# Optimization experiments

Hardware: AMD Instinct MI355X
Metric: run time of the kernel (lower is better)

Reference implementation:

```python
import jax, jax.numpy as jnp
import numpy as np

N_NODES = 10000
N_EDGES = 160000
IN_F = 256
CH = 512
N_LABELS = 1440


def setup_inputs() -> dict:
    key = jax.random.key(0)
    ks = jax.random.split(key, 12)
    x = jax.random.normal(ks[0], (N_NODES, IN_F), dtype=jnp.float32)
    src = jax.random.randint(ks[1], (N_EDGES,), 0, N_NODES)
    dst = jax.random.randint(ks[2], (N_EDGES,), 0, N_NODES)
    s_in = 1.0 / np.sqrt(IN_F)
    s_ch = 1.0 / np.sqrt(CH)
    W1 = jax.random.normal(ks[3], (IN_F, CH), dtype=jnp.float32) * s_in
    V1 = jax.random.normal(ks[4], (IN_F, CH), dtype=jnp.float32) * s_in
    b1 = jnp.zeros((CH,), dtype=jnp.float32)
    Wk = jax.random.normal(ks[5], (6, CH, CH), dtype=jnp.float32) * s_ch
    Vk = jax.random.normal(ks[6], (6, CH, CH), dtype=jnp.float32) * s_ch
    bk = jnp.zeros((6, CH), dtype=jnp.float32)
    Wd = jax.random.normal(ks[7], (CH, N_LABELS), dtype=jnp.float32) * s_ch
    bd = jnp.zeros((N_LABELS,), dtype=jnp.float32)
    return {"x": x, "src": src, "dst": dst, "W1": W1, "V1": V1, "b1": b1,
            "Wk": Wk, "Vk": Vk, "bk": bk, "Wd": Wd, "bd": bd}


def reference(x, src, dst, W1, V1, b1, Wk, Vk, bk, Wd, bd):
    n = x.shape[0]
    ones = jnp.ones(src.shape[0], dtype=x.dtype)
    # degree-normalized adjacency weights: D_out^{-1/2} A D_in^{-1/2}
    deg_out = jnp.maximum(jax.ops.segment_sum(ones, src, num_segments=n), 1.0)
    deg_in = jnp.maximum(jax.ops.segment_sum(ones, dst, num_segments=n), 1.0)
    w = jax.lax.rsqrt(deg_out[src] * deg_in[dst])  # [E]

    def arma_conv(h, W, V, b):
        m = h @ W                                      # dense transform [N, CH]
        msg = w[:, None] * m[dst]                      # gather + scale   [E, CH]
        agg = jax.ops.segment_sum(msg, src, num_segments=n)  # scatter   [N, CH]
        # gcn_activation relu then outer activation relu (idempotent)
        return jax.nn.relu(agg + h @ V + b)

    h = arma_conv(x, W1, V1, b1)
    for i in range(6):  # convs 2..7, fixed small layer count
        h = arma_conv(h, Wk[i], Vk[i], bk[i])
    return h @ Wd + bd
```

## Files before the change

kernel.cpp:

```cpp
#include <hip/hip_runtime.h>
#include <hip/hip_bf16.h>
#include <stdint.h>

#define NN 10000
#define NE 160000
#define INF 256
#define CH 512
#define NL 1440
#define MPAN 158

typedef __bf16 bf16;
typedef __attribute__((ext_vector_type(8))) bf16 bf16x8;
typedef __attribute__((ext_vector_type(4))) float f32x4;


__device__ __forceinline__ void gload16(const void* g, const void* l) {
    auto gp = reinterpret_cast<const __attribute__((address_space(1))) uint32_t*>(
        reinterpret_cast<uintptr_t>(g));
    auto lp = reinterpret_cast<__attribute__((address_space(3))) uint32_t*>(
        reinterpret_cast<uintptr_t>(l));
    __builtin_amdgcn_global_load_lds(gp, lp, 16, 0, 0);
}

__global__ void deg_kernel(const int* __restrict__ src, const int* __restrict__ dst,
                           int* __restrict__ deg_out, int* __restrict__ deg_in) {
    int e = blockIdx.x * 256 + threadIdx.x;
    if (e < NE) {
        atomicAdd(&deg_out[src[e]], 1);
        atomicAdd(&deg_in[dst[e]], 1);
    }
}

__global__ __launch_bounds__(1024) void scan_kernel(const int* __restrict__ deg,
                                                    int* __restrict__ offsets,
                                                    int* __restrict__ cursor) {
    __shared__ int sums[1024];
    const int PER = 10;
    int tid = threadIdx.x;
    int base = tid * PER;
    int local[PER];
    int s = 0;
    #pragma unroll
    for (int i = 0; i < PER; i++) {
        int v = (base + i < NN) ? deg[base + i] : 0;
        local[i] = s;
        s += v;
    }
    sums[tid] = s;
    __syncthreads();
    for (int off = 1; off < 1024; off <<= 1) {
        int v = (tid >= off) ? sums[tid - off] : 0;
        __syncthreads();
        sums[tid] += v;
        __syncthreads();
    }
    int prev = (tid > 0) ? sums[tid - 1] : 0;
    #pragma unroll
    for (int i = 0; i < PER; i++) {
        if (base + i < NN) {
            int o = prev + local[i];
            offsets[base + i] = o;
            cursor[base + i] = o;
        }
    }
    if (tid == 0) offsets[NN] = sums[1023];
}

__global__ void csr_kernel(const int* __restrict__ src, const int* __restrict__ dst,
                           const int* __restrict__ deg_out, const int* __restrict__ deg_in,
                           int* __restrict__ cursor, int2* __restrict__ edge_pk) {
    int e = blockIdx.x * 256 + threadIdx.x;
    if (e < NE) {
        int s = src[e], d = dst[e];
        float dw = (float)max(deg_out[s], 1) * (float)max(deg_in[d], 1);
        float w = rsqrtf(dw);
        int pos = atomicAdd(&cursor[s], 1);
        edge_pk[pos] = make_int2(d, __float_as_int(w));
    }
}

__global__ __launch_bounds__(256) void gather_agg(
    const uint32_t* __restrict__ h32,
    const int* __restrict__ offsets,
    const int2* __restrict__ edge_pk,
    bf16* __restrict__ outA,
    int CHU, int SLOG, int CBASE, int PANCH) {
    int p = blockIdx.x;
    int slice = p & ((1 << SLOG) - 1);
    int grp = p >> SLOG;
    int wid = threadIdx.x >> 6;
    int lane = threadIdx.x & 63;
    int u = grp * 4 + wid;
    if (u >= NN) return;
    int c = slice * 128 + lane * 2;
    int cu = (slice << 6) + lane;

    int beg = offsets[u], end = offsets[u + 1];
    float a0 = 0.f, a1 = 0.f;
    int e = beg;
    for (; e + 3 < end; e += 4) {
        int2 p0 = edge_pk[e], p1 = edge_pk[e + 1];
        int2 p2 = edge_pk[e + 2], p3 = edge_pk[e + 3];
        uint32_t q0 = h32[p0.x * CHU + cu];
        uint32_t q1 = h32[p1.x * CHU + cu];
        uint32_t q2 = h32[p2.x * CHU + cu];
        uint32_t q3 = h32[p3.x * CHU + cu];
        float w0 = __int_as_float(p0.y), w1 = __int_as_float(p1.y);
        float w2 = __int_as_float(p2.y), w3 = __int_as_float(p3.y);
        a0 += w0 * __uint_as_float(q0 << 16);
        a1 += w0 * __uint_as_float(q0 & 0xffff0000u);
        a0 += w1 * __uint_as_float(q1 << 16);
        a1 += w1 * __uint_as_float(q1 & 0xffff0000u);
        a0 += w2 * __uint_as_float(q2 << 16);
        a1 += w2 * __uint_as_float(q2 & 0xffff0000u);
        a0 += w3 * __uint_as_float(q3 << 16);
        a1 += w3 * __uint_as_float(q3 & 0xffff0000u);
    }
    for (; e < end; e++) {
        int2 pe = edge_pk[e];
        uint32_t qv = h32[pe.x * CHU + cu];
        float wt = __int_as_float(pe.y);
        a0 += wt * __uint_as_float(qv << 16);
        a1 += wt * __uint_as_float(qv & 0xffff0000u);
    }

    bf16 h0 = (bf16)a0, h1 = (bf16)a1;
    int row = u & 63, panel = u >> 6;
    int ch = CBASE + (c >> 5), g = (c >> 3) & 3, j = c & 7;
    size_t base = (size_t)panel * PANCH * 2048 + (size_t)ch * 2048 + g * 512 + row * 8 + j;
    uint32_t hw = (uint32_t)__builtin_bit_cast(uint16_t, h0) |
                  ((uint32_t)__builtin_bit_cast(uint16_t, h1) << 16);
    *(uint32_t*)&outA[base] = hw;
}

__global__ void xb_conv(const float* __restrict__ x, bf16* __restrict__ xb) {
    int idx = blockIdx.x * 256 + threadIdx.x;
    if (idx >= NN * 32) return;
    const float* src = x + (size_t)idx * 8;
    float4 v0 = *(const float4*)src;
    float4 v1 = *(const float4*)(src + 4);
    bf16x8 o;
    o[0] = (bf16)v0.x; o[1] = (bf16)v0.y; o[2] = (bf16)v0.z; o[3] = (bf16)v0.w;
    o[4] = (bf16)v1.x; o[5] = (bf16)v1.y; o[6] = (bf16)v1.z; o[7] = (bf16)v1.w;
    *(bf16x8*)&xb[(size_t)idx * 8] = o;
}

__global__ void split_hi(const float* __restrict__ in, bf16* __restrict__ out,
                         int M, int K, int PANCH) {
    int idx = blockIdx.x * 256 + threadIdx.x;
    int K8 = K >> 3;
    if (idx >= M * K8) return;
    int m = idx / K8;
    int k8 = (idx % K8) * 8;
    bf16x8 hi;
    #pragma unroll
    for (int j = 0; j < 8; j++) hi[j] = (bf16)in[(size_t)m * K + k8 + j];
    int panel = m >> 6, row = m & 63;
    int c = k8 >> 5, g = (k8 & 31) >> 3;
    size_t base = ((size_t)panel * PANCH + c) * 2048 + g * 512 + row * 8;
    *(bf16x8*)&out[base] = hi;
}

__global__ void vw_split(const float* __restrict__ V, const float* __restrict__ W,
                         bf16* __restrict__ out, int K,
                         size_t vStride, size_t wStride, size_t outStride) {
    int z = blockIdx.z;
    V += (size_t)z * vStride;
    W += (size_t)z * wStride;
    out += (size_t)z * outStride;
    int idx = blockIdx.x * 256 + threadIdx.x;
    int K8 = K >> 3;
    if (idx >= 512 * K8) return;
    int k8 = (idx / 512) * 8;
    int n = idx % 512;
    int KCh = K >> 5;
    bf16x8 vv, ww;
    #pragma unroll
    for (int j = 0; j < 8; j++) {
        vv[j] = (bf16)V[(size_t)(k8 + j) * 512 + n];
        ww[j] = (bf16)W[(size_t)(k8 + j) * 512 + n];
    }
    int panel = n >> 7, row = n & 127;
    int c = k8 >> 5, g = (k8 & 31) >> 3;
    size_t base = (size_t)panel * (2 * KCh) * 4096 + g * 1024 + row * 8;
    *(bf16x8*)&out[base + (size_t)c * 4096] = vv;
    *(bf16x8*)&out[base + (size_t)(KCh + c) * 4096] = ww;
}

__global__ void tsplit(const float* __restrict__ in, bf16* __restrict__ out,
                       int K, int N) {
    int idx = blockIdx.x * 256 + threadIdx.x;
    int K8 = K >> 3;
    if (idx >= N * K8) return;
    int k8 = (idx / N) * 8;
    int n = idx % N;
    int KCh = K >> 5;
    bf16x8 hi;
    #pragma unroll
    for (int j = 0; j < 8; j++) hi[j] = (bf16)in[(size_t)(k8 + j) * N + n];
    int panel = n >> 7, row = n & 127;
    int c = k8 >> 5, g = (k8 & 31) >> 3;
    size_t base = ((size_t)panel * KCh) * 4096 + g * 1024 + row * 8;
    *(bf16x8*)&out[base + (size_t)c * 4096] = hi;
}

__global__ __launch_bounds__(256, 3) void gemm_layer(
    const bf16* __restrict__ At, const bf16* __restrict__ Bt,
    const float* __restrict__ bias, bf16* __restrict__ hbOut,
    bf16* __restrict__ AtNext, int M, int KCh, int BX) {
    __shared__ bf16 lA[2][2][2048];
    __shared__ bf16 lB[2][2][4096];

    int nwg = gridDim.x;
    int q = nwg >> 3, r = nwg & 7;
    int p = blockIdx.x;
    int xcd = p & 7, slot = p >> 3;
    int L = (xcd < r ? xcd * (q + 1) : r * (q + 1) + (xcd - r) * q) + slot;
    int by = L / BX, bx = L % BX;

    int tid = threadIdx.x;
    int lane = tid & 63, w = tid >> 6;
    int wm = w >> 1, wn = w & 1;
    int lr = lane & 15, lg = lane >> 4;
    const bf16* Ab = At + (size_t)by * KCh * 2048;
    const bf16* Bb = Bt + (size_t)bx * KCh * 4096;

    f32x4 acc[2][4];
    #pragma unroll
    for (int i = 0; i < 2; i++)
        #pragma unroll
        for (int j = 0; j < 4; j++) {
            f32x4 z = {0.f, 0.f, 0.f, 0.f};
            acc[i][j] = z;
        }

    int u0 = tid, u1 = tid + 256;
    int offA = lg * 512 + (wm * 32 + lr) * 8;
    int offB = lg * 1024 + (wn * 64 + lr) * 8;

    #define LSTAGE(bufi, it)                                                      \
        do {                                                                      \
            const bf16* a0 = Ab + (size_t)(2 * (it)) * 2048;                      \
            const bf16* a1 = Ab + (size_t)(2 * (it) + 1) * 2048;                  \
            const bf16* b0 = Bb + (size_t)(2 * (it)) * 4096;                      \
            const bf16* b1 = Bb + (size_t)(2 * (it) + 1) * 4096;                  \
            gload16(a0 + tid * 8, &lA[bufi][0][tid * 8]);                         \
            gload16(a1 + tid * 8, &lA[bufi][1][tid * 8]);                         \
            gload16(b0 + u0 * 8, &lB[bufi][0][u0 * 8]);                           \
            gload16(b0 + u1 * 8, &lB[bufi][0][u1 * 8]);                           \
            gload16(b1 + u0 * 8, &lB[bufi][1][u0 * 8]);                           \
            gload16(b1 + u1 * 8, &lB[bufi][1][u1 * 8]);                           \
        } while (0)

    int NIT = KCh >> 1;
    LSTAGE(0, 0);
    __syncthreads();

    int buf = 0;
    for (int it = 0; it < NIT; it++) {
        if (it + 1 < NIT) LSTAGE(buf ^ 1, it + 1);
        #pragma unroll
        for (int kk = 0; kk < 2; kk++) {
            bf16x8 bh[4];
            #pragma unroll
            for (int n = 0; n < 4; n++)
                bh[n] = *(const bf16x8*)&lB[buf][kk][offB + n * 128];
            #pragma unroll
            for (int m = 0; m < 2; m++) {
                bf16x8 ah = *(const bf16x8*)&lA[buf][kk][offA + m * 128];
                #pragma unroll
                for (int n = 0; n < 4; n++)
                    acc[m][n] = __builtin_amdgcn_mfma_f32_16x16x32_bf16(
                        ah, bh[n], acc[m][n], 0, 0, 0);
            }
        }
        __syncthreads();
        buf ^= 1;
    }
    #undef LSTAGE

    int m0 = by * 64, n0 = bx * 128;
    #pragma unroll
    for (int m = 0; m < 2; m++) {
        #pragma unroll
        for (int n = 0; n < 4; n++) {
            int gr0 = m0 + wm * 32 + m * 16 + lg * 4;
            int gc = n0 + wn * 64 + n * 16 + lr;
            float bv = bias[gc];
            int cch = gc >> 5, g2 = (gc >> 3) & 3, j2 = gc & 7;
            #pragma unroll
            for (int r2 = 0; r2 < 4; r2++) {
                int grow = gr0 + r2;
                if (grow >= M) continue;
                float v = fmaxf(acc[m][n][r2] + bv, 0.f);
                bf16 hv = (bf16)v;
                hbOut[(size_t)grow * 512 + gc] = hv;
                int panel = grow >> 6, row = grow & 63;
                AtNext[(size_t)panel * 32 * 2048 + (size_t)cch * 2048 +
                       g2 * 512 + row * 8 + j2] = hv;
            }
        }
    }
}

__global__ __launch_bounds__(256, 4) void gemm_out(
    const bf16* __restrict__ At, const bf16* __restrict__ Bt,
    float* __restrict__ Fout, const float* __restrict__ bias,
    int M, int N, int KCh, int BX, int PANCH) {
    __shared__ bf16 ldsA[2][2][2048];
    __shared__ bf16 ldsB[2][4096];

    int nwg = gridDim.x;
    int q = nwg >> 3, r = nwg & 7;
    int p = blockIdx.x;
    int xcd = p & 7, slot = p >> 3;
    int L = (xcd < r ? xcd * (q + 1) : r * (q + 1) + (xcd - r) * q) + slot;
    int by = L / BX, bx = L % BX;

    int tid = threadIdx.x;
    int lane = tid & 63, w = tid >> 6;
    int wm = w >> 1, wn = w & 1;
    int lr = lane & 15, lg = lane >> 4;
    const bf16* Ab0 = At + (size_t)(2 * by) * PANCH * 2048;
    const bf16* Ab1 = At + (size_t)(2 * by + 1) * PANCH * 2048;
    const bf16* Bbase = Bt + (size_t)bx * KCh * 4096;

    f32x4 acc[4][4];
    #pragma unroll
    for (int i = 0; i < 4; i++)
        #pragma unroll
        for (int j = 0; j < 4; j++) {
            f32x4 z = {0.f, 0.f, 0.f, 0.f};
            acc[i][j] = z;
        }

    int u0 = tid, u1 = tid + 256;
    int offA = lg * 512 + lr * 8;
    int offB = lg * 1024 + (wn * 64 + lr) * 8;

    #define OSTAGE(bufi, t)                                                       \
        do {                                                                      \
            const bf16* s0h = Ab0 + (size_t)(t) * 2048;                           \
            const bf16* s1h = Ab1 + (size_t)(t) * 2048;                           \
            const bf16* sBh = Bbase + (size_t)(t) * 4096;                         \
            gload16(s0h + tid * 8, &ldsA[bufi][0][tid * 8]);                      \
            gload16(s1h + tid * 8, &ldsA[bufi][1][tid * 8]);                      \
            gload16(sBh + u0 * 8, &ldsB[bufi][u0 * 8]);                           \
            gload16(sBh + u1 * 8, &ldsB[bufi][u1 * 8]);                           \
        } while (0)

    OSTAGE(0, 0);
    __syncthreads();
    int buf = 0;
    for (int t = 0; t < KCh; t++) {
        if (t + 1 < KCh) OSTAGE(buf ^ 1, t + 1);
        bf16x8 bh[4];
        #pragma unroll
        for (int n = 0; n < 4; n++)
            bh[n] = *(const bf16x8*)&ldsB[buf][offB + n * 128];
        #pragma unroll
        for (int m = 0; m < 4; m++) {
            bf16x8 ah = *(const bf16x8*)&ldsA[buf][wm][offA + m * 128];
            #pragma unroll
            for (int n = 0; n < 4; n++)
                acc[m][n] = __builtin_amdgcn_mfma_f32_16x16x32_bf16(ah, bh[n],
                                                                   acc[m][n], 0, 0, 0);
        }
        __syncthreads();
        buf ^= 1;
    }
    #undef OSTAGE

    int m0 = by * 128, n0 = bx * 128;
    #pragma unroll
    for (int m = 0; m < 4; m++)
        #pragma unroll
        for (int n = 0; n < 4; n++) {
            int grow0 = m0 + wm * 64 + m * 16 + lg * 4;
            int gcol = n0 + wn * 64 + n * 16 + lr;
            if (gcol >= N) continue;
            float bv = bias[gcol];
            #pragma unroll
            for (int r2 = 0; r2 < 4; r2++) {
                int grow = grow0 + r2;
                if (grow < M) Fout[(size_t)grow * N + gcol] = acc[m][n][r2] + bv;
            }
        }
}

extern "C" void kernel_launch(void* const* d_in, const int* in_sizes, int n_in,
                              void* d_out, int out_size, void* d_ws, size_t ws_size,
                              hipStream_t stream) {
    const float* x  = (const float*)d_in[0];
    const int* src  = (const int*)d_in[1];
    const int* dst  = (const int*)d_in[2];
    const float* W1 = (const float*)d_in[3];
    const float* V1 = (const float*)d_in[4];
    const float* b1 = (const float*)d_in[5];
    const float* Wk = (const float*)d_in[6];
    const float* Vk = (const float*)d_in[7];
    const float* bk = (const float*)d_in[8];
    const float* Wd = (const float*)d_in[9];
    const float* bd = (const float*)d_in[10];

    int* deg_out  = (int*)d_ws;
    int* deg_in   = deg_out + 10240;
    int* offsets  = deg_in + 10240;
    int* cursor   = offsets + 10240;
    int2* edge_pk = (int2*)(cursor + 10240);
    bf16* A_L1 = (bf16*)(edge_pk + NE);
    bf16* Am0  = A_L1 + (size_t)MPAN * 16 * 2048;
    bf16* Am1  = Am0 + (size_t)MPAN * 32 * 2048;
    bf16* B1t  = Am1 + (size_t)MPAN * 32 * 2048;
    bf16* Bkt  = B1t + (size_t)4 * 16 * 4096;
    bf16* Wdt  = Bkt + (size_t)6 * 4 * 32 * 4096;

    bf16* hb0 = (bf16*)d_out;
    bf16* hb1 = hb0 + (size_t)NN * 512;
    bf16* xb  = hb1 + (size_t)NN * 512;
    float* out = (float*)d_out;

    hipMemsetAsync(deg_out, 0, 2 * 10240 * sizeof(int), stream);
    deg_kernel<<<(NE + 255) / 256, 256, 0, stream>>>(src, dst, deg_out, deg_in);
    scan_kernel<<<1, 1024, 0, stream>>>(deg_out, offsets, cursor);
    csr_kernel<<<(NE + 255) / 256, 256, 0, stream>>>(src, dst, deg_out, deg_in,
                                                     cursor, edge_pk);

    xb_conv<<<1250, 256, 0, stream>>>(x, xb);
    split_hi<<<1250, 256, 0, stream>>>(x, A_L1, NN, INF, 16);
    vw_split<<<dim3(64, 1, 1), 256, 0, stream>>>(V1, W1, B1t, INF, 0, 0, 0);
    vw_split<<<dim3(128, 1, 6), 256, 0, stream>>>(Vk, Wk, Bkt, CH,
                                                  (size_t)CH * 512, (size_t)CH * 512,
                                                  (size_t)4 * 32 * 4096);
    tsplit<<<360, 256, 0, stream>>>(Wd, Wdt, CH, NL);

    dim3 blk(256);
    int glayer = MPAN * 4;
    int gout = (MPAN / 2) * 12;

    gather_agg<<<2 * 2500, blk, 0, stream>>>((const uint32_t*)xb, offsets, edge_pk,
                                             A_L1, 128, 1, 8, 16);
    gemm_layer<<<glayer, blk, 0, stream>>>(A_L1, B1t, b1, hb0, Am0, NN, 16, 4);

    for (int i = 0; i < 6; i++) {
        bf16* hcur = (i & 1) ? hb1 : hb0;
        bf16* hnxt = (i & 1) ? hb0 : hb1;
        bf16* Acur = (i & 1) ? Am1 : Am0;
        bf16* Anxt = (i & 1) ? Am0 : Am1;
        gather_agg<<<4 * 2500, blk, 0, stream>>>((const uint32_t*)hcur, offsets,
                                                 edge_pk, Acur, 256, 2, 16, 32);
        gemm_layer<<<glayer, blk, 0, stream>>>(Acur, Bkt + (size_t)i * 4 * 32 * 4096,
                                               bk + (size_t)i * CH, hnxt, Anxt,
                                               NN, 32, 4);
    }

    gemm_out<<<gout, blk, 0, stream>>>(Am0, Wdt, out, bd, NN, NL, 16, 12, 32);
}
```

Before: 435.7 us.

## Unroll gather by 8, fuse x conversion kernels, double-K-step output GEMM, skip unused write

The gather-aggregate loop now handles 8 edges per iteration so more independent loads are in flight. The two kernels that converted x to bf16 (row-major and panel layout) are merged into one that reads x once and writes both layouts. The output GEMM stages two K-chunks per barrier, which halves the number of syncs but doubles LDS use and lowers launch-bounds occupancy from 4 to 2. The last hidden layer also skips writing its row-major bf16 copy, since nothing reads it.

```diff
diff --git a/kernel.cpp b/kernel.cpp
--- a/kernel.cpp
+++ b/kernel.cpp
@@ -98,23 +98,33 @@
     int beg = offsets[u], end = offsets[u + 1];
     float a0 = 0.f, a1 = 0.f;
     int e = beg;
+    for (; e + 7 < end; e += 8) {
+        int2 pk[8];
+        uint32_t qq[8];
+        #pragma unroll
+        for (int k = 0; k < 8; k++) pk[k] = edge_pk[e + k];
+        #pragma unroll
+        for (int k = 0; k < 8; k++) qq[k] = h32[pk[k].x * CHU + cu];
+        #pragma unroll
+        for (int k = 0; k < 8; k++) {
+            float wt = __int_as_float(pk[k].y);
+            a0 += wt * __uint_as_float(qq[k] << 16);
+            a1 += wt * __uint_as_float(qq[k] & 0xffff0000u);
+        }
+    }
     for (; e + 3 < end; e += 4) {
-        int2 p0 = edge_pk[e], p1 = edge_pk[e + 1];
-        int2 p2 = edge_pk[e + 2], p3 = edge_pk[e + 3];
-        uint32_t q0 = h32[p0.x * CHU + cu];
-        uint32_t q1 = h32[p1.x * CHU + cu];
-        uint32_t q2 = h32[p2.x * CHU + cu];
-        uint32_t q3 = h32[p3.x * CHU + cu];
-        float w0 = __int_as_float(p0.y), w1 = __int_as_float(p1.y);
-        float w2 = __int_as_float(p2.y), w3 = __int_as_float(p3.y);
-        a0 += w0 * __uint_as_float(q0 << 16);
-        a1 += w0 * __uint_as_float(q0 & 0xffff0000u);
-        a0 += w1 * __uint_as_float(q1 << 16);
-        a1 += w1 * __uint_as_float(q1 & 0xffff0000u);
-        a0 += w2 * __uint_as_float(q2 << 16);
-        a1 += w2 * __uint_as_float(q2 & 0xffff0000u);
-        a0 += w3 * __uint_as_float(q3 << 16);
-        a1 += w3 * __uint_as_float(q3 & 0xffff0000u);
+        int2 pk[4];
+        uint32_t qq[4];
+        #pragma unroll
+        for (int k = 0; k < 4; k++) pk[k] = edge_pk[e + k];
+        #pragma unroll
+        for (int k = 0; k < 4; k++) qq[k] = h32[pk[k].x * CHU + cu];
+        #pragma unroll
+        for (int k = 0; k < 4; k++) {
+            float wt = __int_as_float(pk[k].y);
+            a0 += wt * __uint_as_float(qq[k] << 16);
+            a1 += wt * __uint_as_float(qq[k] & 0xffff0000u);
+        }
     }
     for (; e < end; e++) {
         int2 pe = edge_pk[e];
@@ -133,32 +143,22 @@
     *(uint32_t*)&outA[base] = hw;
 }
 
-__global__ void xb_conv(const float* __restrict__ x, bf16* __restrict__ xb) {
+__global__ void x_conv(const float* __restrict__ x, bf16* __restrict__ xb,
+                       bf16* __restrict__ outT) {
     int idx = blockIdx.x * 256 + threadIdx.x;
     if (idx >= NN * 32) return;
-    const float* src = x + (size_t)idx * 8;
+    int m = idx >> 5;
+    int k8 = (idx & 31) * 8;
+    const float* src = x + (size_t)m * INF + k8;
     float4 v0 = *(const float4*)src;
     float4 v1 = *(const float4*)(src + 4);
     bf16x8 o;
     o[0] = (bf16)v0.x; o[1] = (bf16)v0.y; o[2] = (bf16)v0.z; o[3] = (bf16)v0.w;
     o[4] = (bf16)v1.x; o[5] = (bf16)v1.y; o[6] = (bf16)v1.z; o[7] = (bf16)v1.w;
     *(bf16x8*)&xb[(size_t)idx * 8] = o;
-}
-
-__global__ void split_hi(const float* __restrict__ in, bf16* __restrict__ out,
-                         int M, int K, int PANCH) {
-    int idx = blockIdx.x * 256 + threadIdx.x;
-    int K8 = K >> 3;
-    if (idx >= M * K8) return;
-    int m = idx / K8;
-    int k8 = (idx % K8) * 8;
-    bf16x8 hi;
-    #pragma unroll
-    for (int j = 0; j < 8; j++) hi[j] = (bf16)in[(size_t)m * K + k8 + j];
     int panel = m >> 6, row = m & 63;
     int c = k8 >> 5, g = (k8 & 31) >> 3;
-    size_t base = ((size_t)panel * PANCH + c) * 2048 + g * 512 + row * 8;
-    *(bf16x8*)&out[base] = hi;
+    *(bf16x8*)&outT[((size_t)panel * 16 + c) * 2048 + g * 512 + row * 8] = o;
 }
 
 __global__ void vw_split(const float* __restrict__ V, const float* __restrict__ W,
@@ -294,7 +294,7 @@
                 if (grow >= M) continue;
                 float v = fmaxf(acc[m][n][r2] + bv, 0.f);
                 bf16 hv = (bf16)v;
-                hbOut[(size_t)grow * 512 + gc] = hv;
+                if (hbOut) hbOut[(size_t)grow * 512 + gc] = hv;
                 int panel = grow >> 6, row = grow & 63;
                 AtNext[(size_t)panel * 32 * 2048 + (size_t)cch * 2048 +
                        g2 * 512 + row * 8 + j2] = hv;
@@ -303,12 +303,12 @@
     }
 }
 
-__global__ __launch_bounds__(256, 4) void gemm_out(
+__global__ __launch_bounds__(256, 2) void gemm_out(
     const bf16* __restrict__ At, const bf16* __restrict__ Bt,
     float* __restrict__ Fout, const float* __restrict__ bias,
     int M, int N, int KCh, int BX, int PANCH) {
-    __shared__ bf16 ldsA[2][2][2048];
-    __shared__ bf16 ldsB[2][4096];
+    __shared__ bf16 ldsA[2][2][2][2048];
+    __shared__ bf16 ldsB[2][2][4096];
 
     int nwg = gridDim.x;
     int q = nwg >> 3, r = nwg & 7;
@@ -338,33 +338,39 @@
     int offA = lg * 512 + lr * 8;
     int offB = lg * 1024 + (wn * 64 + lr) * 8;
 
-    #define OSTAGE(bufi, t)                                                       \
+    #define OSTAGE(bufi, it)                                                      \
         do {                                                                      \
-            const bf16* s0h = Ab0 + (size_t)(t) * 2048;                           \
-            const bf16* s1h = Ab1 + (size_t)(t) * 2048;                           \
-            const bf16* sBh = Bbase + (size_t)(t) * 4096;                         \
-            gload16(s0h + tid * 8, &ldsA[bufi][0][tid * 8]);                      \
-            gload16(s1h + tid * 8, &ldsA[bufi][1][tid * 8]);                      \
-            gload16(sBh + u0 * 8, &ldsB[bufi][u0 * 8]);                           \
-            gload16(sBh + u1 * 8, &ldsB[bufi][u1 * 8]);                           \
+            _Pragma("unroll") for (int kk = 0; kk < 2; kk++) {                    \
+                const bf16* s0 = Ab0 + (size_t)(2 * (it) + kk) * 2048;            \
+                const bf16* s1 = Ab1 + (size_t)(2 * (it) + kk) * 2048;            \
+                const bf16* sB = Bbase + (size_t)(2 * (it) + kk) * 4096;          \
+                gload16(s0 + tid * 8, &ldsA[bufi][kk][0][tid * 8]);               \
+                gload16(s1 + tid * 8, &ldsA[bufi][kk][1][tid * 8]);               \
+                gload16(sB + u0 * 8, &ldsB[bufi][kk][u0 * 8]);                    \
+                gload16(sB + u1 * 8, &ldsB[bufi][kk][u1 * 8]);                    \
+            }                                                                     \
         } while (0)
 
+    int NIT = KCh >> 1;
     OSTAGE(0, 0);
     __syncthreads();
     int buf = 0;
-    for (int t = 0; t < KCh; t++) {
-        if (t + 1 < KCh) OSTAGE(buf ^ 1, t + 1);
-        bf16x8 bh[4];
-        #pragma unroll
-        for (int n = 0; n < 4; n++)
-            bh[n] = *(const bf16x8*)&ldsB[buf][offB + n * 128];
-        #pragma unroll
-        for (int m = 0; m < 4; m++) {
-            bf16x8 ah = *(const bf16x8*)&ldsA[buf][wm][offA + m * 128];
+    for (int it = 0; it < NIT; it++) {
+        if (it + 1 < NIT) OSTAGE(buf ^ 1, it + 1);
+        #pragma unroll
+        for (int kk = 0; kk < 2; kk++) {
+            bf16x8 bh[4];
             #pragma unroll
             for (int n = 0; n < 4; n++)
-                acc[m][n] = __builtin_amdgcn_mfma_f32_16x16x32_bf16(ah, bh[n],
-                                                                   acc[m][n], 0, 0, 0);
+                bh[n] = *(const bf16x8*)&ldsB[buf][kk][offB + n * 128];
+            #pragma unroll
+            for (int m = 0; m < 4; m++) {
+                bf16x8 ah = *(const bf16x8*)&ldsA[buf][kk][wm][offA + m * 128];
+                #pragma unroll
+                for (int n = 0; n < 4; n++)
+                    acc[m][n] = __builtin_amdgcn_mfma_f32_16x16x32_bf16(
+                        ah, bh[n], acc[m][n], 0, 0, 0);
+            }
         }
         __syncthreads();
         buf ^= 1;
@@ -426,8 +432,7 @@
     csr_kernel<<<(NE + 255) / 256, 256, 0, stream>>>(src, dst, deg_out, deg_in,
                                                      cursor, edge_pk);
 
-    xb_conv<<<1250, 256, 0, stream>>>(x, xb);
-    split_hi<<<1250, 256, 0, stream>>>(x, A_L1, NN, INF, 16);
+    x_conv<<<1250, 256, 0, stream>>>(x, xb, A_L1);
     vw_split<<<dim3(64, 1, 1), 256, 0, stream>>>(V1, W1, B1t, INF, 0, 0, 0);
     vw_split<<<dim3(128, 1, 6), 256, 0, stream>>>(Vk, Wk, Bkt, CH,
                                                   (size_t)CH * 512, (size_t)CH * 512,
@@ -450,7 +455,8 @@
         gather_agg<<<4 * 2500, blk, 0, stream>>>((const uint32_t*)hcur, offsets,
                                                  edge_pk, Acur, 256, 2, 16, 32);
         gemm_layer<<<glayer, blk, 0, stream>>>(Acur, Bkt + (size_t)i * 4 * 32 * 4096,
-                                               bk + (size_t)i * CH, hnxt, Anxt,
+                                               bk + (size_t)i * CH,
+                                               (i == 5) ? nullptr : hnxt, Anxt,
                                                NN, 32, 4);
     }
 
```

Measured after the change: 388.3 us. -10.9%, faster.
